# Optimization experiments

Measured on AMD Instinct MI355X. Metric: run time of the kernel, lower is better.

## Reference

```python
import jax, jax.numpy as jnp
import numpy as np

B, C, P, H, W = 64, 2048, 4, 14, 14
HID = C * P // 2  # 4096
S = H * W         # 196


def setup_inputs() -> dict:
    key = jax.random.key(0)
    k1, k2, k3, k4, k5 = jax.random.split(key, 5)
    x = jax.random.normal(k1, (B, C, H, W), dtype=jnp.float32)
    w1 = jax.random.normal(k2, (HID, C), dtype=jnp.float32) * 0.02
    b1 = jnp.zeros((HID,), dtype=jnp.float32)
    w2 = jax.random.normal(k3, (C * P, HID), dtype=jnp.float32) * 0.02
    b2 = jnp.zeros((C * P,), dtype=jnp.float32)
    return {"x": x, "w1": w1, "b1": b1, "w2": w2, "b2": b2}


def reference(x, w1, b1, w2, b2):
    # SE-style gating: global average pool -> fc1 -> sigmoid -> fc2 -> sigmoid
    g = x.mean(axis=(2, 3))                                  # [B, C]
    h = jax.nn.sigmoid(g @ w1.T + b1)                        # [B, HID]
    w = jax.nn.sigmoid(h @ w2.T + b2).reshape(B, P, C)       # grouping_result [B, P, C]
    # Weighted feature: mean over channels of w[b,p,c] * x[b,c,s].
    # Original materializes [B,P,C,196] then AdaptiveAvgPool3d over C;
    # mathematically this is a batched matmul divided by C.
    xs = x.reshape(B, C, S)                                  # [B, C, 196]
    feat = jnp.einsum('bpc,bcs->bps', w, xs) / C             # [B, P, 196]
    return (w, feat.reshape(B, P, H, W))
```

## Files before the change

### kernel.cpp

```cpp
#include <hip/hip_runtime.h>
#include <hip/hip_bf16.h>
#include <cstdint>
#include <cstddef>

typedef __attribute__((ext_vector_type(4))) float  f32x4;
typedef __attribute__((ext_vector_type(8))) short  short8;

typedef __attribute__((address_space(3))) uint32_t as3_u32;
typedef __attribute__((address_space(1))) uint32_t as1_u32;

__device__ __forceinline__ short f2bf(float f) {
  __hip_bfloat16 h = __float2bfloat16(f);
  return *reinterpret_cast<short*>(&h);
}
__device__ __forceinline__ float sigmoidf(float x) {
  return 1.0f / (1.0f + __expf(-x));
}

__global__ __launch_bounds__(256) void pool_kernel(const float* __restrict__ x,
                                                   short* __restrict__ g) {
  __shared__ float sums[784];
  const int tid = threadIdx.x;
  const f32x4* base = (const f32x4*)(x + (size_t)blockIdx.x * (16 * 196));
#pragma unroll
  for (int it = 0; it < 4; ++it) {
    int i = it * 256 + tid;
    if (it < 3 || tid < 16) {
      f32x4 v = base[i];
      sums[i] = v[0] + v[1] + v[2] + v[3];
    }
  }
  __syncthreads();
  if (tid < 16) {
    float s = 0.f;
#pragma unroll
    for (int j = 0; j < 49; ++j) s += sums[tid * 49 + j];
    g[blockIdx.x * 16 + tid] = f2bf(s * (1.0f / 196.0f));
  }
}

template<int N, int K, int WAVES, bool OUT_BF16>
__device__ __forceinline__ void gemm_body(const short* __restrict__ A,
                                          const float* __restrict__ B,
                                          const float* __restrict__ bias,
                                          void* __restrict__ outp,
                                          float* __restrict__ red) {
  constexpr int KW = K / WAVES;
  constexpr int NK = KW / 32;
  constexpr int NT = WAVES * 64;
  const int n0  = blockIdx.x * 16;
  const int tid = threadIdx.x;
  const int l   = tid & 63;
  const int wv  = tid >> 6;
  const int kw0 = wv * KW;

  const int ko = (l >> 4) * 8;
  const float* Bp = B + (size_t)(n0 + (l & 15)) * K + kw0 + ko;
  const short* Ap = A + (size_t)(l & 15) * K + kw0 + ko;

  f32x4 acc0 = {}, acc1 = {}, acc2 = {}, acc3 = {};

  f32x4 bc0 = *(const f32x4*)(Bp);
  f32x4 bc1 = *(const f32x4*)(Bp + 4);
  short8 ac0 = *(const short8*)(Ap);
  short8 ac1 = *(const short8*)(Ap + 16 * K);
  short8 ac2 = *(const short8*)(Ap + 32 * K);
  short8 ac3 = *(const short8*)(Ap + 48 * K);

  for (int t = 0; t < NK; ++t) {
    f32x4 bn0 = {}, bn1 = {};
    short8 an0 = {}, an1 = {}, an2 = {}, an3 = {};
    if (t + 1 < NK) {
      const float* bp = Bp + (t + 1) * 32;
      const short* ap = Ap + (t + 1) * 32;
      bn0 = *(const f32x4*)(bp);
      bn1 = *(const f32x4*)(bp + 4);
      an0 = *(const short8*)(ap);
      an1 = *(const short8*)(ap + 16 * K);
      an2 = *(const short8*)(ap + 32 * K);
      an3 = *(const short8*)(ap + 48 * K);
    }
    short8 bb;
    bb[0] = f2bf(bc0[0]); bb[1] = f2bf(bc0[1]); bb[2] = f2bf(bc0[2]); bb[3] = f2bf(bc0[3]);
    bb[4] = f2bf(bc1[0]); bb[5] = f2bf(bc1[1]); bb[6] = f2bf(bc1[2]); bb[7] = f2bf(bc1[3]);
    acc0 = __builtin_amdgcn_mfma_f32_16x16x32_bf16(ac0, bb, acc0, 0, 0, 0);
    acc1 = __builtin_amdgcn_mfma_f32_16x16x32_bf16(ac1, bb, acc1, 0, 0, 0);
    acc2 = __builtin_amdgcn_mfma_f32_16x16x32_bf16(ac2, bb, acc2, 0, 0, 0);
    acc3 = __builtin_amdgcn_mfma_f32_16x16x32_bf16(ac3, bb, acc3, 0, 0, 0);
    bc0 = bn0; bc1 = bn1;
    ac0 = an0; ac1 = an1; ac2 = an2; ac3 = an3;
  }

  {
    float* rw = red + wv * 1024;
    const int mb = (l >> 4) << 2;
    const int nn = l & 15;
#pragma unroll
    for (int r = 0; r < 4; ++r) rw[(0  + mb + r) * 16 + nn] = acc0[r];
#pragma unroll
    for (int r = 0; r < 4; ++r) rw[(16 + mb + r) * 16 + nn] = acc1[r];
#pragma unroll
    for (int r = 0; r < 4; ++r) rw[(32 + mb + r) * 16 + nn] = acc2[r];
#pragma unroll
    for (int r = 0; r < 4; ++r) rw[(48 + mb + r) * 16 + nn] = acc3[r];
  }
  __syncthreads();

#pragma unroll
  for (int i = tid; i < 1024; i += NT) {
    float s = 0.f;
#pragma unroll
    for (int w = 0; w < WAVES; ++w) s += red[w * 1024 + i];
    int m  = i >> 4;
    int nn = n0 + (i & 15);
    s = sigmoidf(s + bias[nn]);
    if constexpr (OUT_BF16) ((short*)outp)[(size_t)m * N + nn] = f2bf(s);
    else                    ((float*)outp)[(size_t)m * N + nn] = s;
  }
}

__global__ __launch_bounds__(1024, 4) void gemm1_kernel(const short* __restrict__ A,
                                                        const float* __restrict__ B,
                                                        const float* __restrict__ bias,
                                                        short* __restrict__ outp) {
  __shared__ float red[16 * 1024];
  gemm_body<4096, 2048, 16, true>(A, B, bias, outp, red);
}

__global__ __launch_bounds__(512, 6) void gemm2_kernel(const short* __restrict__ A,
                                                       const float* __restrict__ B,
                                                       const float* __restrict__ bias,
                                                       float* __restrict__ outp,
                                                       float* __restrict__ zbuf) {
  constexpr int N = 8192, K = 4096;
  __shared__ float lds[12288];
  const int tid = threadIdx.x;
  const int l   = tid & 63;
  const int wv  = tid >> 6;
  const int n0  = blockIdx.x * 16;

  if (tid < 98) zbuf[blockIdx.x * 98 + tid] = 0.f;

  const char*  gB = (const char*)B + (size_t)n0 * (K * 4);
  const short* Ap = A + (size_t)(l & 15) * K + ((l >> 4) << 3);

#define G2_STAGE(c_, b_)                                                       \
  {                                                                            \
    _Pragma("unroll")                                                          \
    for (int j = 0; j < 2; ++j) {                                              \
      int idx = j * 512 + tid;                                                 \
      int r   = idx >> 6;                                                      \
      int d   = (idx & 63) << 4;                                               \
      int s   = d ^ ((r & 7) << 4);                                            \
      const char* src = gB + (size_t)r * (K * 4) + (size_t)(c_) * 1024 + s;    \
      char* dst = (char*)lds + (size_t)(b_) * 16384 +                          \
                  (size_t)(j * 512 + (tid & ~63)) * 16;                        \
      __builtin_amdgcn_global_load_lds((as1_u32*)src, (as3_u32*)dst, 16, 0, 0);\
    }                                                                          \
  }
#define G2_LOADA(c_, ar_)                                                      \
  {                                                                            \
    const short* ap = Ap + (c_) * 256 + wv * 32;                               \
    _Pragma("unroll")                                                          \
    for (int f = 0; f < 4; ++f)                                                \
      ar_[f] = *(const short8*)(ap + (size_t)f * 16 * K);                      \
  }

  f32x4 acc0 = {}, acc1 = {}, acc2 = {}, acc3 = {};
  short8 aC[4], aN[4];

  G2_STAGE(0, 0);
  __builtin_amdgcn_sched_barrier(0);
  G2_LOADA(0, aC);
  __builtin_amdgcn_sched_barrier(0);
  G2_STAGE(1, 1);
  __builtin_amdgcn_sched_barrier(0);

  const int row = l & 15;
  const int swz = (row & 7) << 4;
  const int rb  = row * 1024;
  const int kb  = (wv << 7) + ((l >> 4) << 5);

  int s0i = 0, s1i = 1, s2i = 2;

#pragma unroll 1
  for (int c = 0; c < 16; ++c) {
    if (c < 15) { asm volatile("s_waitcnt vmcnt(6)" ::: "memory"); }
    else        { asm volatile("s_waitcnt vmcnt(4)" ::: "memory"); }
    __builtin_amdgcn_sched_barrier(0);
    __builtin_amdgcn_s_barrier();
    __builtin_amdgcn_sched_barrier(0);
    if (c + 1 < 16) { G2_LOADA(c + 1, aN); }
    __builtin_amdgcn_sched_barrier(0);
    if (c + 2 < 16) { G2_STAGE(c + 2, s2i); }
    __builtin_amdgcn_sched_barrier(0);

    const char* bufc = (const char*)lds + (size_t)s0i * 16384;
    f32x4 b0 = *(const f32x4*)(bufc + rb + ((kb)      ^ swz));
    f32x4 b1 = *(const f32x4*)(bufc + rb + ((kb + 16) ^ swz));
    short8 bb;
    bb[0] = f2bf(b0[0]); bb[1] = f2bf(b0[1]); bb[2] = f2bf(b0[2]); bb[3] = f2bf(b0[3]);
    bb[4] = f2bf(b1[0]); bb[5] = f2bf(b1[1]); bb[6] = f2bf(b1[2]); bb[7] = f2bf(b1[3]);
    acc0 = __builtin_amdgcn_mfma_f32_16x16x32_bf16(aC[0], bb, acc0, 0, 0, 0);
    acc1 = __builtin_amdgcn_mfma_f32_16x16x32_bf16(aC[1], bb, acc1, 0, 0, 0);
    acc2 = __builtin_amdgcn_mfma_f32_16x16x32_bf16(aC[2], bb, acc2, 0, 0, 0);
    acc3 = __builtin_amdgcn_mfma_f32_16x16x32_bf16(aC[3], bb, acc3, 0, 0, 0);

    if (c + 1 < 16) {
#pragma unroll
      for (int f = 0; f < 4; ++f) aC[f] = aN[f];
    }
    int t = s0i; s0i = s1i; s1i = s2i; s2i = t;
  }

  __syncthreads();
  float* red = lds;
  {
    float* rw = red + wv * 1024;
    const int mb = (l >> 4) << 2;
    const int nn = l & 15;
#pragma unroll
    for (int r = 0; r < 4; ++r) rw[(0  + mb + r) * 16 + nn] = acc0[r];
#pragma unroll
    for (int r = 0; r < 4; ++r) rw[(16 + mb + r) * 16 + nn] = acc1[r];
#pragma unroll
    for (int r = 0; r < 4; ++r) rw[(32 + mb + r) * 16 + nn] = acc2[r];
#pragma unroll
    for (int r = 0; r < 4; ++r) rw[(48 + mb + r) * 16 + nn] = acc3[r];
  }
  __syncthreads();
#pragma unroll
  for (int i = tid; i < 1024; i += 512) {
    float s = 0.f;
#pragma unroll
    for (int w = 0; w < 8; ++w) s += red[w * 1024 + i];
    int m  = i >> 4;
    int nn = n0 + (i & 15);
    outp[(size_t)m * N + nn] = sigmoidf(s + bias[nn]);
  }
#undef G2_STAGE
#undef G2_LOADA
}

__global__ __launch_bounds__(256) void einsum_kernel(const float* __restrict__ x,
                                                     const float* __restrict__ wg,
                                                     float* __restrict__ feat) {
  const int b   = blockIdx.x >> 4;
  const int cc  = blockIdx.x & 15;
  const int tid = threadIdx.x;
  if (tid >= 196) return;
  const float* wp = wg + (size_t)b * 8192 + cc * 128;
  const float* xp = x + (size_t)b * 2048 * 196 + (size_t)cc * 128 * 196 + tid;
  float a0 = 0.f, a1 = 0.f, a2 = 0.f, a3 = 0.f;
#pragma unroll 8
  for (int c = 0; c < 128; ++c) {
    float xv = xp[(size_t)c * 196];
    a0 = __builtin_fmaf(wp[c],        xv, a0);
    a1 = __builtin_fmaf(wp[2048 + c], xv, a1);
    a2 = __builtin_fmaf(wp[4096 + c], xv, a2);
    a3 = __builtin_fmaf(wp[6144 + c], xv, a3);
  }
  const float invC = 1.0f / 2048.0f;
  atomicAdd(feat + (b * 4 + 0) * 196 + tid, a0 * invC);
  atomicAdd(feat + (b * 4 + 1) * 196 + tid, a1 * invC);
  atomicAdd(feat + (b * 4 + 2) * 196 + tid, a2 * invC);
  atomicAdd(feat + (b * 4 + 3) * 196 + tid, a3 * invC);
}

extern "C" void kernel_launch(void* const* d_in, const int* in_sizes, int n_in,
                              void* d_out, int out_size, void* d_ws, size_t ws_size,
                              hipStream_t stream) {
  const float* x  = (const float*)d_in[0];
  const float* w1 = (const float*)d_in[1];
  const float* b1 = (const float*)d_in[2];
  const float* w2 = (const float*)d_in[3];
  const float* b2 = (const float*)d_in[4];
  float* out = (float*)d_out;

  short* g_bf = (short*)d_ws;
  short* h_bf = g_bf + 64 * 2048;

  float* wout = out;
  float* feat = out + 524288;

  pool_kernel<<<8192, 256, 0, stream>>>(x, g_bf);

  gemm1_kernel<<<4096 / 16, 1024, 0, stream>>>(g_bf, w1, b1, h_bf);

  gemm2_kernel<<<512, 512, 0, stream>>>(h_bf, w2, b2, wout, feat);

  einsum_kernel<<<64 * 16, 256, 0, stream>>>(x, wout, feat);
}
```

Before: 94.96 us.

## Pre-cast w2 to bf16 in a separate kernel and use a bf16 gemm2

Adds a kernel that converts the fp32 w2 matrix to bf16 in workspace on every call, plus a new gemm2 variant that streams the bf16 weights into LDS with a 3-stage swizzled buffer. This halves the bytes gemm2 itself reads and removes in-kernel conversion. The cost is that the cast pass reads the full fp32 w2 and writes a bf16 copy, so total memory traffic for w2 goes up. The new path runs only when the workspace is large enough; otherwise it falls back to the old fp32 gemm2.

```diff
diff --git a/kernel.cpp b/kernel.cpp
--- a/kernel.cpp
+++ b/kernel.cpp
@@ -5,6 +5,7 @@
 
 typedef __attribute__((ext_vector_type(4))) float  f32x4;
 typedef __attribute__((ext_vector_type(8))) short  short8;
+typedef __attribute__((ext_vector_type(4))) short  short4v;
 
 typedef __attribute__((address_space(3))) uint32_t as3_u32;
 typedef __attribute__((address_space(1))) uint32_t as1_u32;
@@ -37,6 +38,18 @@
     for (int j = 0; j < 49; ++j) s += sums[tid * 49 + j];
     g[blockIdx.x * 16 + tid] = f2bf(s * (1.0f / 196.0f));
   }
+}
+
+__global__ __launch_bounds__(256) void cast_w2_kernel(const float* __restrict__ w2,
+                                                      short* __restrict__ w2bf) {
+  const size_t g = (size_t)blockIdx.x * 256 + threadIdx.x;
+  const float* src = w2 + g * 8;
+  f32x4 a = *(const f32x4*)(src);
+  f32x4 b = *(const f32x4*)(src + 4);
+  short8 o;
+  o[0] = f2bf(a[0]); o[1] = f2bf(a[1]); o[2] = f2bf(a[2]); o[3] = f2bf(a[3]);
+  o[4] = f2bf(b[0]); o[5] = f2bf(b[1]); o[6] = f2bf(b[2]); o[7] = f2bf(b[3]);
+  *(short8*)(w2bf + g * 8) = o;
 }
 
 template<int N, int K, int WAVES, bool OUT_BF16>
@@ -127,11 +140,128 @@
   gemm_body<4096, 2048, 16, true>(A, B, bias, outp, red);
 }
 
-__global__ __launch_bounds__(512, 6) void gemm2_kernel(const short* __restrict__ A,
-                                                       const float* __restrict__ B,
-                                                       const float* __restrict__ bias,
-                                                       float* __restrict__ outp,
-                                                       float* __restrict__ zbuf) {
+__global__ __launch_bounds__(512, 6) void gemm2_bf16(const short* __restrict__ A,
+                                                     const short* __restrict__ Bbf,
+                                                     const float* __restrict__ bias,
+                                                     float* __restrict__ outp,
+                                                     float* __restrict__ zbuf) {
+  constexpr int N = 8192, K = 4096;
+  __shared__ char ldsb[49152];
+  const int tid = threadIdx.x;
+  const int l   = tid & 63;
+  const int wv  = tid >> 6;
+  const int n0  = blockIdx.x * 16;
+
+  if (tid < 98) zbuf[blockIdx.x * 98 + tid] = 0.f;
+
+  const char*  gB = (const char*)Bbf + (size_t)n0 * (K * 2);
+  const short* Ap = A + (size_t)(l & 15) * K + ((l >> 4) << 3);
+
+#define G2B_STAGE(c_, b_)                                                      \
+  {                                                                            \
+    _Pragma("unroll")                                                          \
+    for (int j = 0; j < 2; ++j) {                                              \
+      int idx = j * 512 + tid;                                                 \
+      int r   = idx >> 6;                                                      \
+      int d   = (idx & 63) << 4;                                               \
+      int s   = d ^ ((r & 7) << 4);                                            \
+      const char* src = gB + (size_t)r * (K * 2) + (size_t)(c_) * 1024 + s;    \
+      char* dst = (char*)ldsb + (size_t)(b_) * 16384 +                         \
+                  (size_t)(j * 512 + (tid & ~63)) * 16;                        \
+      __builtin_amdgcn_global_load_lds((as1_u32*)src, (as3_u32*)dst, 16, 0, 0);\
+    }                                                                          \
+  }
+#define G2B_LOADA(c_, ar_)                                                     \
+  {                                                                            \
+    const short* ap = Ap + (c_) * 512 + wv * 64;                               \
+    _Pragma("unroll")                                                          \
+    for (int t = 0; t < 2; ++t) {                                              \
+      _Pragma("unroll")                                                        \
+      for (int f = 0; f < 4; ++f)                                              \
+        ar_[t * 4 + f] = *(const short8*)(ap + t * 32 + (size_t)f * 16 * K);   \
+    }                                                                          \
+  }
+
+  f32x4 acc0 = {}, acc1 = {}, acc2 = {}, acc3 = {};
+  short8 aC[8], aN[8];
+
+  G2B_STAGE(0, 0);
+  __builtin_amdgcn_sched_barrier(0);
+  G2B_LOADA(0, aC);
+  __builtin_amdgcn_sched_barrier(0);
+  G2B_STAGE(1, 1);
+  __builtin_amdgcn_sched_barrier(0);
+
+  const int row = l & 15;
+  const int swz = (row & 7) << 4;
+  const int rb  = row * 1024;
+
+  int s0i = 0, s1i = 1, s2i = 2;
+
+#pragma unroll 1
+  for (int c = 0; c < 8; ++c) {
+    if (c < 7) { asm volatile("s_waitcnt vmcnt(10)" ::: "memory"); }
+    else       { asm volatile("s_waitcnt vmcnt(8)"  ::: "memory"); }
+    __builtin_amdgcn_sched_barrier(0);
+    __builtin_amdgcn_s_barrier();
+    __builtin_amdgcn_sched_barrier(0);
+    if (c + 1 < 8) { G2B_LOADA(c + 1, aN); }
+    __builtin_amdgcn_sched_barrier(0);
+    if (c + 2 < 8) { G2B_STAGE(c + 2, s2i); }
+    __builtin_amdgcn_sched_barrier(0);
+
+    const char* bufc = ldsb + (size_t)s0i * 16384;
+#pragma unroll
+    for (int t = 0; t < 2; ++t) {
+      const int kb = (wv << 7) + (t << 6) + ((l >> 4) << 4);
+      short8 bb = *(const short8*)(bufc + rb + (kb ^ swz));
+      acc0 = __builtin_amdgcn_mfma_f32_16x16x32_bf16(aC[t * 4 + 0], bb, acc0, 0, 0, 0);
+      acc1 = __builtin_amdgcn_mfma_f32_16x16x32_bf16(aC[t * 4 + 1], bb, acc1, 0, 0, 0);
+      acc2 = __builtin_amdgcn_mfma_f32_16x16x32_bf16(aC[t * 4 + 2], bb, acc2, 0, 0, 0);
+      acc3 = __builtin_amdgcn_mfma_f32_16x16x32_bf16(aC[t * 4 + 3], bb, acc3, 0, 0, 0);
+    }
+
+    if (c + 1 < 8) {
+#pragma unroll
+      for (int f = 0; f < 8; ++f) aC[f] = aN[f];
+    }
+    int t2 = s0i; s0i = s1i; s1i = s2i; s2i = t2;
+  }
+
+  __syncthreads();
+  float* red = (float*)ldsb;
+  {
+    float* rw = red + wv * 1024;
+    const int mb = (l >> 4) << 2;
+    const int nn = l & 15;
+#pragma unroll
+    for (int r = 0; r < 4; ++r) rw[(0  + mb + r) * 16 + nn] = acc0[r];
+#pragma unroll
+    for (int r = 0; r < 4; ++r) rw[(16 + mb + r) * 16 + nn] = acc1[r];
+#pragma unroll
+    for (int r = 0; r < 4; ++r) rw[(32 + mb + r) * 16 + nn] = acc2[r];
+#pragma unroll
+    for (int r = 0; r < 4; ++r) rw[(48 + mb + r) * 16 + nn] = acc3[r];
+  }
+  __syncthreads();
+#pragma unroll
+  for (int i = tid; i < 1024; i += 512) {
+    float s = 0.f;
+#pragma unroll
+    for (int w = 0; w < 8; ++w) s += red[w * 1024 + i];
+    int m  = i >> 4;
+    int nn = n0 + (i & 15);
+    outp[(size_t)m * N + nn] = sigmoidf(s + bias[nn]);
+  }
+#undef G2B_STAGE
+#undef G2B_LOADA
+}
+
+__global__ __launch_bounds__(512, 6) void gemm2_f32(const short* __restrict__ A,
+                                                    const float* __restrict__ B,
+                                                    const float* __restrict__ bias,
+                                                    float* __restrict__ outp,
+                                                    float* __restrict__ zbuf) {
   constexpr int N = 8192, K = 4096;
   __shared__ float lds[12288];
   const int tid = threadIdx.x;
@@ -277,17 +407,25 @@
   const float* b2 = (const float*)d_in[4];
   float* out = (float*)d_out;
 
-  short* g_bf = (short*)d_ws;
-  short* h_bf = g_bf + 64 * 2048;
+  short* g_bf  = (short*)d_ws;
+  short* h_bf  = g_bf + 64 * 2048;
+  short* w2_bf = (short*)((char*)d_ws + (1 << 20));
+
+  const bool use_cast = ws_size >= ((size_t)(1 << 20) + 67108864ULL);
 
   float* wout = out;
   float* feat = out + 524288;
 
-  pool_kernel<<<8192, 256, 0, stream>>>(x, g_bf);
+  pool_kernel<<<(64 * 2048) / 16, 256, 0, stream>>>(x, g_bf);
 
   gemm1_kernel<<<4096 / 16, 1024, 0, stream>>>(g_bf, w1, b1, h_bf);
 
-  gemm2_kernel<<<512, 512, 0, stream>>>(h_bf, w2, b2, wout, feat);
+  if (use_cast) {
+    cast_w2_kernel<<<16384, 256, 0, stream>>>(w2, w2_bf);
+    gemm2_bf16<<<512, 512, 0, stream>>>(h_bf, w2_bf, b2, wout, feat);
+  } else {
+    gemm2_f32<<<512, 512, 0, stream>>>(h_bf, w2, b2, wout, feat);
+  }
 
   einsum_kernel<<<64 * 16, 256, 0, stream>>>(x, wout, feat);
 }
```

Result: slower. 138.8 us (+46.2%).
